# Performance work log

Measured on AMD Instinct MI355X. Metric: run time of the kernel, lower is better.

The kernel has to match this reference:

```python
import jax, jax.numpy as jnp
import numpy as np

B, T, C, H = 4, 4096, 1024, 16

def setup_inputs() -> dict:
    key = jax.random.key(0)
    k1, k2, k3, k4 = jax.random.split(key, 4)
    return {
        "x": jax.random.normal(k1, (B, T, C), dtype=jnp.float32),
        "W_attn": jax.random.normal(k2, (C, C), dtype=jnp.float32) * 0.02,
        "b_attn": jnp.zeros((C,), dtype=jnp.float32),
        "W_proj": jax.random.normal(k3, (C, C), dtype=jnp.float32) * 0.02,
        "b_proj": jnp.zeros((C,), dtype=jnp.float32),
        "temp": jnp.ones((H, 1), dtype=jnp.float32),
        "n_head": H,
    }

def reference(x, W_attn, b_attn, W_proj, b_proj, temp, n_head):
    Bb, Tt, Cc = x.shape
    D = Cc // n_head
    # c_attn (torch Linear: x @ W.T + b)
    w = x @ W_attn.T + b_attn                         # (B,T,C)
    w = w.reshape(Bb, Tt, n_head, D).transpose(0, 2, 1, 3)  # (B,H,T,D)
    # F.normalize over token axis (dim=-2), eps=1e-12
    norm = jnp.maximum(jnp.sqrt(jnp.sum(w * w, axis=-2, keepdims=True)), 1e-12)
    w_normed = w / norm
    tmp = jnp.sum(w_normed ** 2, axis=-1) * temp      # (B,H,T) * (H,1) -> (B,H,T)
    Pi = jax.nn.softmax(tmp, axis=1)                  # softmax over heads
    Pi_prob = Pi / (jnp.sum(Pi, axis=-1, keepdims=True) + 1e-8)  # (B,H,T)
    dots = jnp.einsum('bht,bhtd->bhd', Pi_prob, w ** 2)          # (B,H,D)
    attn = 1.0 / (1.0 + dots)                         # (B,H,D)
    y = -(w * Pi[..., None]) * attn[:, :, None, :]    # (B,H,T,D)
    y = y.transpose(0, 2, 1, 3).reshape(Bb, Tt, Cc)
    return y @ W_proj.T + b_proj
```

## Files before the change

kernel.cpp:

```cpp
#include <hip/hip_runtime.h>
#include <hip/hip_bf16.h>

#define BB 4
#define TT 4096
#define CC 1024
#define HH 16
#define DD 64

typedef __attribute__((ext_vector_type(8))) short short8;
typedef __attribute__((ext_vector_type(8))) __bf16 bf16x8;
typedef __attribute__((ext_vector_type(4))) float f32x4;

static __device__ __forceinline__ unsigned short f2bf(float f) {
    unsigned int u = __builtin_bit_cast(unsigned int, f);
    unsigned int r = (u + 0x7FFFu + ((u >> 16) & 1u)) >> 16;
    return (unsigned short)r;
}
static __device__ __forceinline__ float bf2f(unsigned short h) {
    return __builtin_bit_cast(float, ((unsigned int)h) << 16);
}

__global__ void k_f32_to_bf16(const float* __restrict__ src,
                              unsigned short* __restrict__ dst, int n4) {
    int i = blockIdx.x * 256 + threadIdx.x;
    if (i >= n4) return;
    float4 v = ((const float4*)src)[i];
    ushort4 o;
    o.x = f2bf(v.x); o.y = f2bf(v.y); o.z = f2bf(v.z); o.w = f2bf(v.w);
    ((ushort4*)dst)[i] = o;
}

#define GBM 256
#define GBN 256
#define GBK 32

static __device__ __forceinline__ void stage_tile32(
    const unsigned short* __restrict__ Gbase, unsigned short* lbase,
    int k0, int K, int wave, int lane)
{
    #pragma unroll
    for (int q = 0; q < 2; ++q) {
        int c = (wave * 2 + q) * 64 + lane;
        int r = c >> 2;
        int j = c & 3;
        int srcj = (j - (r >> 1)) & 3;
        const unsigned short* g = Gbase + (size_t)r * K + k0 + srcj * 8;
        __builtin_amdgcn_global_load_lds(
            (const __attribute__((address_space(1))) void*)g,
            (__attribute__((address_space(3))) void*)(lbase + (wave * 2 + q) * 512),
            16, 0, 0);
    }
}

template<int MODE>
__global__ __launch_bounds__(512, 2)
void k_gemm256(const unsigned short* __restrict__ A,
               const unsigned short* __restrict__ B,
               const float* __restrict__ bias,
               void* __restrict__ Cout,
               float* __restrict__ S,
               int M, int N, int K)
{
    __shared__ unsigned short lds[4][16384];
    const int tid  = threadIdx.x;
    const int wave = tid >> 6;
    const int lane = tid & 63;
    const int wr = wave >> 2;
    const int wc = wave & 3;
    const int fr = lane & 15;
    const int hi = lane >> 4;

    const int wg  = blockIdx.x;
    const int swz = (wg & 7) * 32 + (wg >> 3);
    const int bn  = swz & 3;
    const int bm  = swz >> 2;
    const int b   = bm >> 4;

    const unsigned short* Abase = A + (size_t)(bm * GBM) * K;
    const unsigned short* Bbase = B +
        ((size_t)((MODE == 1 ? b * N : 0) + bn * GBN)) * K;

    const int nt = K / GBK;

    const int sl   = (hi + (fr >> 1)) & 3;
    const int aoff = (wr * 128 + fr) * 32 + sl * 8;
    const int boff = 8192 + (wc * 64 + fr) * 32 + sl * 8;

    f32x4 acc[8][4] = {};

    stage_tile32(Abase, lds[0],        0,       K, wave, lane);
    stage_tile32(Bbase, lds[0] + 8192, 0,       K, wave, lane);
    stage_tile32(Abase, lds[1],        GBK,     K, wave, lane);
    stage_tile32(Bbase, lds[1] + 8192, GBK,     K, wave, lane);
    stage_tile32(Abase, lds[2],        2 * GBK, K, wave, lane);
    stage_tile32(Bbase, lds[2] + 8192, 2 * GBK, K, wave, lane);

    for (int kt = 0; kt < nt; ++kt) {
        const unsigned short* buf = lds[kt & 3];
        unsigned short* sbuf = lds[(kt + 3) & 3];
        int k3 = kt + 3; if (k3 >= nt) k3 = nt - 1;

        asm volatile("s_waitcnt vmcnt(8)" ::: "memory");
        __builtin_amdgcn_s_barrier();

        short8 af[8], bfr[4];
        #pragma unroll
        for (int i = 0; i < 4; ++i) bfr[i] = *(const short8*)&buf[boff + i * 512];
        #pragma unroll
        for (int i = 0; i < 8; ++i) af[i] = *(const short8*)&buf[aoff + i * 512];

        stage_tile32(Abase, sbuf, k3 * GBK, K, wave, lane);
        stage_tile32(Bbase, sbuf + 8192, k3 * GBK, K, wave, lane);

        __builtin_amdgcn_s_setprio(1);
        #pragma unroll
        for (int mi = 0; mi < 8; ++mi)
            #pragma unroll
            for (int ni = 0; ni < 4; ++ni)
                acc[mi][ni] = __builtin_amdgcn_mfma_f32_16x16x32_bf16(
                    __builtin_bit_cast(bf16x8, af[mi]),
                    __builtin_bit_cast(bf16x8, bfr[ni]),
                    acc[mi][ni], 0, 0, 0);
        __builtin_amdgcn_s_setprio(0);
    }

    __syncthreads();

    const int cg = fr;
    const int rg = hi * 4;
    float* sblk = (float*)&lds[0][0];
    if (MODE == 0) {
        if (tid < GBN) sblk[tid] = 0.f;
        __syncthreads();
    }
    float csum[4] = {};
    #pragma unroll
    for (int mi = 0; mi < 8; ++mi) {
        #pragma unroll
        for (int ni = 0; ni < 4; ++ni) {
            int col = bn * GBN + wc * 64 + ni * 16 + cg;
            float bv = bias[col];
            #pragma unroll
            for (int j = 0; j < 4; ++j) {
                int row = bm * GBM + wr * 128 + mi * 16 + rg + j;
                float v = acc[mi][ni][j] + bv;
                if (MODE == 0) {
                    ((unsigned short*)Cout)[(size_t)row * N + col] = f2bf(v);
                    csum[ni] += v * v;
                } else {
                    ((float*)Cout)[(size_t)row * N + col] = v;
                }
            }
        }
    }
    if (MODE == 0) {
        #pragma unroll
        for (int ni = 0; ni < 4; ++ni)
            atomicAdd(&sblk[wc * 64 + ni * 16 + cg], csum[ni]);
        __syncthreads();
        if (tid < GBN) atomicAdd(&S[b * CC + bn * GBN + tid], sblk[tid]);
    }
}

__global__ __launch_bounds__(256)
void k_row_softmax(unsigned short* __restrict__ w16, const float* __restrict__ S,
                   const float* __restrict__ temp,
                   float* __restrict__ dotsU, float* __restrict__ sumPi)
{
    __shared__ float dots_local[CC];
    __shared__ float sPi_local[HH];
    const int tid  = threadIdx.x;
    const int wave = tid >> 6;
    const int lane = tid & 63;
    const int bb   = blockIdx.x >> 7;
    const int tile = blockIdx.x & 127;

    for (int c = tid; c < CC; c += 256) dots_local[c] = 0.f;
    if (tid < HH) sPi_local[tid] = 0.f;
    __syncthreads();

    const int g3 = lane >> 3;
    const int li = lane & 7;

    float inv[2][8], tsc[2];
    #pragma unroll
    for (int q = 0; q < 2; ++q) {
        int c = q * 512 + lane * 8;
        const float4* sp = (const float4*)&S[bb * CC + c];
        float4 s0 = sp[0], s1 = sp[1];
        inv[q][0] = 1.f / fmaxf(s0.x, 1e-24f); inv[q][1] = 1.f / fmaxf(s0.y, 1e-24f);
        inv[q][2] = 1.f / fmaxf(s0.z, 1e-24f); inv[q][3] = 1.f / fmaxf(s0.w, 1e-24f);
        inv[q][4] = 1.f / fmaxf(s1.x, 1e-24f); inv[q][5] = 1.f / fmaxf(s1.y, 1e-24f);
        inv[q][6] = 1.f / fmaxf(s1.z, 1e-24f); inv[q][7] = 1.f / fmaxf(s1.w, 1e-24f);
        tsc[q] = temp[q * 8 + g3];
    }

    float dacc[2][8] = {};
    float sPiAcc[2] = {};

    for (int i = 0; i < 8; ++i) {
        int t = tile * 32 + wave * 8 + i;
        unsigned short* row = w16 + ((size_t)bb * TT + t) * CC;
        float wf[2][8];
        float pq[2];
        #pragma unroll
        for (int q = 0; q < 2; ++q) {
            short8 v = *(const short8*)&row[q * 512 + lane * 8];
            float s = 0.f;
            #pragma unroll
            for (int j = 0; j < 8; ++j) {
                wf[q][j] = bf2f((unsigned short)v[j]);
                s += wf[q][j] * wf[q][j] * inv[q][j];
            }
            pq[q] = s;
        }
        #pragma unroll
        for (int off = 1; off < 8; off <<= 1) {
            pq[0] += __shfl_xor(pq[0], off);
            pq[1] += __shfl_xor(pq[1], off);
        }
        pq[0] *= tsc[0]; pq[1] *= tsc[1];
        float mx = fmaxf(pq[0], pq[1]);
        mx = fmaxf(mx, __shfl_xor(mx, 8));
        mx = fmaxf(mx, __shfl_xor(mx, 16));
        mx = fmaxf(mx, __shfl_xor(mx, 32));
        float e0 = __expf(pq[0] - mx), e1 = __expf(pq[1] - mx);
        float ss = e0 + e1;
        ss += __shfl_xor(ss, 8);
        ss += __shfl_xor(ss, 16);
        ss += __shfl_xor(ss, 32);
        float rs = 1.f / ss;
        float piv[2] = { e0 * rs, e1 * rs };
        #pragma unroll
        for (int q = 0; q < 2; ++q) {
            short8 yo;
            #pragma unroll
            for (int j = 0; j < 8; ++j) {
                dacc[q][j] += piv[q] * wf[q][j] * wf[q][j];
                yo[j] = (short)f2bf(-wf[q][j] * piv[q]);
            }
            *(short8*)&row[q * 512 + lane * 8] = yo;
            if (li == 0) sPiAcc[q] += piv[q];
        }
    }

    #pragma unroll
    for (int q = 0; q < 2; ++q) {
        int c = q * 512 + lane * 8;
        #pragma unroll
        for (int j = 0; j < 8; ++j)
            atomicAdd(&dots_local[c + j], dacc[q][j]);
        if (li == 0) atomicAdd(&sPi_local[q * 8 + g3], sPiAcc[q]);
    }
    __syncthreads();
    for (int c = tid; c < CC; c += 256) atomicAdd(&dotsU[bb * CC + c], dots_local[c]);
    if (tid < HH) atomicAdd(&sumPi[bb * HH + tid], sPi_local[tid]);
}

__global__ void k_scale_wproj(const float* __restrict__ Wp,
                              const float* __restrict__ dotsU,
                              const float* __restrict__ sumPi,
                              unsigned short* __restrict__ out)
{
    int i = blockIdx.x * 256 + threadIdx.x;
    int bq  = i >> 18;
    int rem = i & 262143;
    int n   = rem >> 8;
    int cg  = (rem & 255) * 4;
    float4 wv = *(const float4*)&Wp[n * CC + cg];
    float4 du = *(const float4*)&dotsU[bq * CC + cg];
    float sp = sumPi[bq * HH + (cg >> 6)] + 1e-8f;
    float a0 = 1.f / (1.f + du.x / sp);
    float a1 = 1.f / (1.f + du.y / sp);
    float a2 = 1.f / (1.f + du.z / sp);
    float a3 = 1.f / (1.f + du.w / sp);
    ushort4 o;
    o.x = f2bf(wv.x * a0); o.y = f2bf(wv.y * a1);
    o.z = f2bf(wv.z * a2); o.w = f2bf(wv.w * a3);
    *(ushort4*)&out[((size_t)bq * CC + n) * CC + cg] = o;
}

extern "C" void kernel_launch(void* const* d_in, const int* in_sizes, int n_in,
                              void* d_out, int out_size, void* d_ws, size_t ws_size,
                              hipStream_t stream) {
    const float* x      = (const float*)d_in[0];
    const float* W_attn = (const float*)d_in[1];
    const float* b_attn = (const float*)d_in[2];
    const float* W_proj = (const float*)d_in[3];
    const float* b_proj = (const float*)d_in[4];
    const float* temp   = (const float*)d_in[5];

    unsigned short* xb = (unsigned short*)d_out;

    char* ws = (char*)d_ws;
    unsigned short* w16   = (unsigned short*)(ws);
    unsigned short* Wa16  = (unsigned short*)(ws + 33554432);
    unsigned short* Wp16b = (unsigned short*)(ws + 35651584);
    float* S     = (float*)(ws + 44040192);
    float* dotsU = (float*)(ws + 44056576);
    float* sumPi = (float*)(ws + 44072960);

    k_f32_to_bf16<<<dim3(16384), dim3(256), 0, stream>>>(x, xb, 4194304);
    k_f32_to_bf16<<<dim3(1024), dim3(256), 0, stream>>>(W_attn, Wa16, 262144);

    hipMemsetAsync(S, 0, 16384 + 16384 + 256, stream);

    k_gemm256<0><<<dim3(256), dim3(512), 0, stream>>>(
        xb, Wa16, b_attn, w16, S, BB * TT, CC, CC);

    k_row_softmax<<<dim3(512), dim3(256), 0, stream>>>(w16, S, temp, dotsU, sumPi);

    k_scale_wproj<<<dim3(4096), dim3(256), 0, stream>>>(W_proj, dotsU, sumPi, Wp16b);

    k_gemm256<1><<<dim3(256), dim3(512), 0, stream>>>(
        w16, Wp16b, b_proj, d_out, nullptr, BB * TT, CC, CC);
}
```

Measured before the change: 129.8 us.

## Shrink GEMM tile to 128x256 with 3-stage pipeline and fuse input conversions

Halves the GEMM M tile from 256 to 128 rows, which doubles the grid to 512 workgroups so all CUs get work. The LDS ring goes from 4 to 3 buffers and prefetch depth from 3 to 2 stages, with the wait count adjusted to match, and launch bounds now allow 4 blocks per CU. The two fp32-to-bf16 conversion launches are merged into one. The trade-off is less data reuse per tile and a shallower prefetch that may expose more memory latency.

```diff
diff --git a/kernel.cpp b/kernel.cpp
--- a/kernel.cpp
+++ b/kernel.cpp
@@ -20,21 +20,24 @@
     return __builtin_bit_cast(float, ((unsigned int)h) << 16);
 }
 
-__global__ void k_f32_to_bf16(const float* __restrict__ src,
-                              unsigned short* __restrict__ dst, int n4) {
+__global__ void k_convert2(const float* __restrict__ x, unsigned short* __restrict__ xb,
+                           const float* __restrict__ Wa, unsigned short* __restrict__ wab) {
     int i = blockIdx.x * 256 + threadIdx.x;
-    if (i >= n4) return;
-    float4 v = ((const float4*)src)[i];
+    const float* src; unsigned short* dst; int idx;
+    if (i < 4194304) { src = x;  dst = xb;  idx = i; }
+    else             { src = Wa; dst = wab; idx = i - 4194304; }
+    float4 v = ((const float4*)src)[idx];
     ushort4 o;
     o.x = f2bf(v.x); o.y = f2bf(v.y); o.z = f2bf(v.z); o.w = f2bf(v.w);
-    ((ushort4*)dst)[i] = o;
-}
-
-#define GBM 256
+    ((ushort4*)dst)[idx] = o;
+}
+
+#define GBM 128
 #define GBN 256
 #define GBK 32
-
-static __device__ __forceinline__ void stage_tile32(
+#define SLAB 12288
+
+static __device__ __forceinline__ void stage_b(
     const unsigned short* __restrict__ Gbase, unsigned short* lbase,
     int k0, int K, int wave, int lane)
 {
@@ -52,16 +55,31 @@
     }
 }
 
+static __device__ __forceinline__ void stage_a(
+    const unsigned short* __restrict__ Gbase, unsigned short* lbase,
+    int k0, int K, int wave, int lane)
+{
+    int c = wave * 64 + lane;
+    int r = c >> 2;
+    int j = c & 3;
+    int srcj = (j - (r >> 1)) & 3;
+    const unsigned short* g = Gbase + (size_t)r * K + k0 + srcj * 8;
+    __builtin_amdgcn_global_load_lds(
+        (const __attribute__((address_space(1))) void*)g,
+        (__attribute__((address_space(3))) void*)(lbase + wave * 512),
+        16, 0, 0);
+}
+
 template<int MODE>
-__global__ __launch_bounds__(512, 2)
-void k_gemm256(const unsigned short* __restrict__ A,
+__global__ __launch_bounds__(512, 4)
+void k_gemm128(const unsigned short* __restrict__ A,
                const unsigned short* __restrict__ B,
                const float* __restrict__ bias,
                void* __restrict__ Cout,
                float* __restrict__ S,
                int M, int N, int K)
 {
-    __shared__ unsigned short lds[4][16384];
+    __shared__ unsigned short lds[3][SLAB];
     const int tid  = threadIdx.x;
     const int wave = tid >> 6;
     const int lane = tid & 63;
@@ -71,10 +89,10 @@
     const int hi = lane >> 4;
 
     const int wg  = blockIdx.x;
-    const int swz = (wg & 7) * 32 + (wg >> 3);
+    const int swz = (wg & 7) * 64 + (wg >> 3);
     const int bn  = swz & 3;
     const int bm  = swz >> 2;
-    const int b   = bm >> 4;
+    const int b   = bm >> 5;
 
     const unsigned short* Abase = A + (size_t)(bm * GBM) * K;
     const unsigned short* Bbase = B +
@@ -83,38 +101,37 @@
     const int nt = K / GBK;
 
     const int sl   = (hi + (fr >> 1)) & 3;
-    const int aoff = (wr * 128 + fr) * 32 + sl * 8;
-    const int boff = 8192 + (wc * 64 + fr) * 32 + sl * 8;
-
-    f32x4 acc[8][4] = {};
-
-    stage_tile32(Abase, lds[0],        0,       K, wave, lane);
-    stage_tile32(Bbase, lds[0] + 8192, 0,       K, wave, lane);
-    stage_tile32(Abase, lds[1],        GBK,     K, wave, lane);
-    stage_tile32(Bbase, lds[1] + 8192, GBK,     K, wave, lane);
-    stage_tile32(Abase, lds[2],        2 * GBK, K, wave, lane);
-    stage_tile32(Bbase, lds[2] + 8192, 2 * GBK, K, wave, lane);
-
+    const int aoff = (wr * 64 + fr) * 32 + sl * 8;
+    const int boff = 4096 + (wc * 64 + fr) * 32 + sl * 8;
+
+    f32x4 acc[4][4] = {};
+
+    stage_a(Abase, lds[0],        0,   K, wave, lane);
+    stage_b(Bbase, lds[0] + 4096, 0,   K, wave, lane);
+    stage_a(Abase, lds[1],        GBK, K, wave, lane);
+    stage_b(Bbase, lds[1] + 4096, GBK, K, wave, lane);
+
+    int rb = 0;
     for (int kt = 0; kt < nt; ++kt) {
-        const unsigned short* buf = lds[kt & 3];
-        unsigned short* sbuf = lds[(kt + 3) & 3];
-        int k3 = kt + 3; if (k3 >= nt) k3 = nt - 1;
-
-        asm volatile("s_waitcnt vmcnt(8)" ::: "memory");
+        const unsigned short* buf = lds[rb];
+        const int wb = (rb == 0) ? 2 : rb - 1;
+        int k2 = kt + 2; if (k2 >= nt) k2 = nt - 1;
+
+        asm volatile("s_waitcnt vmcnt(3)" ::: "memory");
         __builtin_amdgcn_s_barrier();
 
-        short8 af[8], bfr[4];
+        short8 af[4], bfr[4];
         #pragma unroll
         for (int i = 0; i < 4; ++i) bfr[i] = *(const short8*)&buf[boff + i * 512];
         #pragma unroll
-        for (int i = 0; i < 8; ++i) af[i] = *(const short8*)&buf[aoff + i * 512];
-
-        stage_tile32(Abase, sbuf, k3 * GBK, K, wave, lane);
-        stage_tile32(Bbase, sbuf + 8192, k3 * GBK, K, wave, lane);
+        for (int i = 0; i < 4; ++i) af[i]  = *(const short8*)&buf[aoff + i * 512];
+
+        stage_a(Abase, lds[wb],        k2 * GBK, K, wave, lane);
+        stage_b(Bbase, lds[wb] + 4096, k2 * GBK, K, wave, lane);
 
         __builtin_amdgcn_s_setprio(1);
         #pragma unroll
-        for (int mi = 0; mi < 8; ++mi)
+        for (int mi = 0; mi < 4; ++mi)
             #pragma unroll
             for (int ni = 0; ni < 4; ++ni)
                 acc[mi][ni] = __builtin_amdgcn_mfma_f32_16x16x32_bf16(
@@ -122,6 +139,8 @@
                     __builtin_bit_cast(bf16x8, bfr[ni]),
                     acc[mi][ni], 0, 0, 0);
         __builtin_amdgcn_s_setprio(0);
+
+        rb = (rb == 2) ? 0 : rb + 1;
     }
 
     __syncthreads();
@@ -135,14 +154,14 @@
     }
     float csum[4] = {};
     #pragma unroll
-    for (int mi = 0; mi < 8; ++mi) {
+    for (int mi = 0; mi < 4; ++mi) {
         #pragma unroll
         for (int ni = 0; ni < 4; ++ni) {
             int col = bn * GBN + wc * 64 + ni * 16 + cg;
             float bv = bias[col];
             #pragma unroll
             for (int j = 0; j < 4; ++j) {
-                int row = bm * GBM + wr * 128 + mi * 16 + rg + j;
+                int row = bm * GBM + wr * 64 + mi * 16 + rg + j;
                 float v = acc[mi][ni][j] + bv;
                 if (MODE == 0) {
                     ((unsigned short*)Cout)[(size_t)row * N + col] = f2bf(v);
@@ -300,18 +319,17 @@
     float* dotsU = (float*)(ws + 44056576);
     float* sumPi = (float*)(ws + 44072960);
 
-    k_f32_to_bf16<<<dim3(16384), dim3(256), 0, stream>>>(x, xb, 4194304);
-    k_f32_to_bf16<<<dim3(1024), dim3(256), 0, stream>>>(W_attn, Wa16, 262144);
+    k_convert2<<<dim3(17408), dim3(256), 0, stream>>>(x, xb, W_attn, Wa16);
 
     hipMemsetAsync(S, 0, 16384 + 16384 + 256, stream);
 
-    k_gemm256<0><<<dim3(256), dim3(512), 0, stream>>>(
+    k_gemm128<0><<<dim3(512), dim3(512), 0, stream>>>(
         xb, Wa16, b_attn, w16, S, BB * TT, CC, CC);
 
     k_row_softmax<<<dim3(512), dim3(256), 0, stream>>>(w16, S, temp, dotsU, sumPi);
 
     k_scale_wproj<<<dim3(4096), dim3(256), 0, stream>>>(W_proj, dotsU, sumPi, Wp16b);
 
-    k_gemm256<1><<<dim3(256), dim3(512), 0, stream>>>(
+    k_gemm128<1><<<dim3(512), dim3(512), 0, stream>>>(
         w16, Wp16b, b_proj, d_out, nullptr, BB * TT, CC, CC);
 }
```

After: 135.3 us. 4.3% more time.

## Fuse fp32-to-bf16 conversion of x into first GEMM's A-tile loads

Applied to the files above, without the earlier changes.

Drops the separate kernel that converted x to bf16. The first GEMM now streams fp32 x tiles straight into LDS with a swizzled layout and converts them to bf16 in registers before the MFMAs. This removes a full read and write pass over the 64MB activation. In exchange, the GEMM A-tile traffic doubles, LDS per slab grows, and the pipeline depth drops from 4 to 3 stages, which may expose more load latency in that GEMM.

```diff
diff --git a/kernel.cpp b/kernel.cpp
--- a/kernel.cpp
+++ b/kernel.cpp
@@ -18,6 +18,12 @@
 }
 static __device__ __forceinline__ float bf2f(unsigned short h) {
     return __builtin_bit_cast(float, ((unsigned int)h) << 16);
+}
+static __device__ __forceinline__ bf16x8 cvt8(f32x4 a, f32x4 b) {
+    bf16x8 r;
+    r[0] = (__bf16)a[0]; r[1] = (__bf16)a[1]; r[2] = (__bf16)a[2]; r[3] = (__bf16)a[3];
+    r[4] = (__bf16)b[0]; r[5] = (__bf16)b[1]; r[6] = (__bf16)b[2]; r[7] = (__bf16)b[3];
+    return r;
 }
 
 __global__ void k_f32_to_bf16(const float* __restrict__ src,
@@ -34,7 +40,7 @@
 #define GBN 256
 #define GBK 32
 
-static __device__ __forceinline__ void stage_tile32(
+static __device__ __forceinline__ void stage_b16(
     const unsigned short* __restrict__ Gbase, unsigned short* lbase,
     int k0, int K, int wave, int lane)
 {
@@ -52,16 +58,37 @@
     }
 }
 
+static __device__ __forceinline__ void stage_a32(
+    const float* __restrict__ Gbase, unsigned short* lbase,
+    int k0, int K, int wave, int lane)
+{
+    #pragma unroll
+    for (int q = 0; q < 4; ++q) {
+        int c = q * 512 + wave * 64 + lane;
+        int r = c >> 3;
+        int j = c & 7;
+        int srcj = (j - r) & 7;
+        const float* g = Gbase + (size_t)r * K + k0 + srcj * 4;
+        __builtin_amdgcn_global_load_lds(
+            (const __attribute__((address_space(1))) void*)g,
+            (__attribute__((address_space(3))) void*)(lbase + (q * 512 + wave * 64) * 8),
+            16, 0, 0);
+    }
+}
+
 template<int MODE>
 __global__ __launch_bounds__(512, 2)
-void k_gemm256(const unsigned short* __restrict__ A,
+void k_gemm256(const void* __restrict__ Asrc,
                const unsigned short* __restrict__ B,
                const float* __restrict__ bias,
                void* __restrict__ Cout,
                float* __restrict__ S,
                int M, int N, int K)
 {
-    __shared__ unsigned short lds[4][16384];
+    constexpr int NSLAB  = (MODE == 0) ? 3 : 4;
+    constexpr int SLABSZ = (MODE == 0) ? 24576 : 16384;
+    constexpr int BOFF0  = (MODE == 0) ? 16384 : 8192;
+    __shared__ unsigned short lds[NSLAB][SLABSZ];
     const int tid  = threadIdx.x;
     const int wave = tid >> 6;
     const int lane = tid & 63;
@@ -76,41 +103,76 @@
     const int bm  = swz >> 2;
     const int b   = bm >> 4;
 
-    const unsigned short* Abase = A + (size_t)(bm * GBM) * K;
+    const float* Af32 = (const float*)Asrc + (size_t)(bm * GBM) * K;
+    const unsigned short* Ab16 = (const unsigned short*)Asrc + (size_t)(bm * GBM) * K;
     const unsigned short* Bbase = B +
         ((size_t)((MODE == 1 ? b * N : 0) + bn * GBN)) * K;
 
     const int nt = K / GBK;
 
-    const int sl   = (hi + (fr >> 1)) & 3;
-    const int aoff = (wr * 128 + fr) * 32 + sl * 8;
-    const int boff = 8192 + (wc * 64 + fr) * 32 + sl * 8;
+    const int slB  = (hi + (fr >> 1)) & 3;
+    const int aoff = (wr * 128 + fr) * 32 + slB * 8;
+    const int boff = BOFF0 + (wc * 64 + fr) * 32 + slB * 8;
+    const int sl0   = (2 * hi + fr) & 7;
+    const int sl1   = (2 * hi + 1 + fr) & 7;
+    const int arowf = (wr * 128 + fr) * 32;
 
     f32x4 acc[8][4] = {};
 
-    stage_tile32(Abase, lds[0],        0,       K, wave, lane);
-    stage_tile32(Bbase, lds[0] + 8192, 0,       K, wave, lane);
-    stage_tile32(Abase, lds[1],        GBK,     K, wave, lane);
-    stage_tile32(Bbase, lds[1] + 8192, GBK,     K, wave, lane);
-    stage_tile32(Abase, lds[2],        2 * GBK, K, wave, lane);
-    stage_tile32(Bbase, lds[2] + 8192, 2 * GBK, K, wave, lane);
-
+    if (MODE == 0) {
+        stage_a32(Af32, lds[0],         0,   K, wave, lane);
+        stage_b16(Bbase, lds[0] + BOFF0, 0,   K, wave, lane);
+        stage_a32(Af32, lds[1],         GBK, K, wave, lane);
+        stage_b16(Bbase, lds[1] + BOFF0, GBK, K, wave, lane);
+    } else {
+        stage_b16(Ab16, lds[0],         0,       K, wave, lane);
+        stage_b16(Bbase, lds[0] + BOFF0, 0,       K, wave, lane);
+        stage_b16(Ab16, lds[1],         GBK,     K, wave, lane);
+        stage_b16(Bbase, lds[1] + BOFF0, GBK,     K, wave, lane);
+        stage_b16(Ab16, lds[2],         2 * GBK, K, wave, lane);
+        stage_b16(Bbase, lds[2] + BOFF0, 2 * GBK, K, wave, lane);
+    }
+
+    int rb = 0;
     for (int kt = 0; kt < nt; ++kt) {
-        const unsigned short* buf = lds[kt & 3];
-        unsigned short* sbuf = lds[(kt + 3) & 3];
-        int k3 = kt + 3; if (k3 >= nt) k3 = nt - 1;
-
-        asm volatile("s_waitcnt vmcnt(8)" ::: "memory");
+        const unsigned short* buf;
+        unsigned short* sbuf;
+        int ks;
+        if (MODE == 0) {
+            buf  = lds[rb];
+            sbuf = lds[(rb == 0) ? 2 : rb - 1];
+            ks = kt + 2; if (ks >= nt) ks = nt - 1;
+            asm volatile("s_waitcnt vmcnt(6)" ::: "memory");
+        } else {
+            buf  = lds[kt & 3];
+            sbuf = lds[(kt + 3) & 3];
+            ks = kt + 3; if (ks >= nt) ks = nt - 1;
+            asm volatile("s_waitcnt vmcnt(8)" ::: "memory");
+        }
         __builtin_amdgcn_s_barrier();
 
-        short8 af[8], bfr[4];
+        bf16x8 af[8]; short8 bfr[4];
         #pragma unroll
         for (int i = 0; i < 4; ++i) bfr[i] = *(const short8*)&buf[boff + i * 512];
-        #pragma unroll
-        for (int i = 0; i < 8; ++i) af[i] = *(const short8*)&buf[aoff + i * 512];
-
-        stage_tile32(Abase, sbuf, k3 * GBK, K, wave, lane);
-        stage_tile32(Bbase, sbuf + 8192, k3 * GBK, K, wave, lane);
+        if (MODE == 0) {
+            const float* fbuf = (const float*)buf;
+            #pragma unroll
+            for (int mi = 0; mi < 8; ++mi)
+                af[mi] = cvt8(*(const f32x4*)&fbuf[arowf + mi * 512 + sl0 * 4],
+                              *(const f32x4*)&fbuf[arowf + mi * 512 + sl1 * 4]);
+        } else {
+            #pragma unroll
+            for (int mi = 0; mi < 8; ++mi)
+                af[mi] = __builtin_bit_cast(bf16x8, *(const short8*)&buf[aoff + mi * 512]);
+        }
+
+        if (MODE == 0) {
+            stage_a32(Af32, sbuf,         ks * GBK, K, wave, lane);
+            stage_b16(Bbase, sbuf + BOFF0, ks * GBK, K, wave, lane);
+        } else {
+            stage_b16(Ab16, sbuf,         ks * GBK, K, wave, lane);
+            stage_b16(Bbase, sbuf + BOFF0, ks * GBK, K, wave, lane);
+        }
 
         __builtin_amdgcn_s_setprio(1);
         #pragma unroll
@@ -118,10 +180,11 @@
             #pragma unroll
             for (int ni = 0; ni < 4; ++ni)
                 acc[mi][ni] = __builtin_amdgcn_mfma_f32_16x16x32_bf16(
-                    __builtin_bit_cast(bf16x8, af[mi]),
-                    __builtin_bit_cast(bf16x8, bfr[ni]),
+                    af[mi], __builtin_bit_cast(bf16x8, bfr[ni]),
                     acc[mi][ni], 0, 0, 0);
         __builtin_amdgcn_s_setprio(0);
+
+        rb = (rb == (NSLAB - 1)) ? 0 : rb + 1;
     }
 
     __syncthreads();
@@ -290,8 +353,6 @@
     const float* b_proj = (const float*)d_in[4];
     const float* temp   = (const float*)d_in[5];
 
-    unsigned short* xb = (unsigned short*)d_out;
-
     char* ws = (char*)d_ws;
     unsigned short* w16   = (unsigned short*)(ws);
     unsigned short* Wa16  = (unsigned short*)(ws + 33554432);
@@ -300,13 +361,12 @@
     float* dotsU = (float*)(ws + 44056576);
     float* sumPi = (float*)(ws + 44072960);
 
-    k_f32_to_bf16<<<dim3(16384), dim3(256), 0, stream>>>(x, xb, 4194304);
     k_f32_to_bf16<<<dim3(1024), dim3(256), 0, stream>>>(W_attn, Wa16, 262144);
 
     hipMemsetAsync(S, 0, 16384 + 16384 + 256, stream);
 
     k_gemm256<0><<<dim3(256), dim3(512), 0, stream>>>(
-        xb, Wa16, b_attn, w16, S, BB * TT, CC, CC);
+        x, Wa16, b_attn, w16, S, BB * TT, CC, CC);
 
     k_row_softmax<<<dim3(512), dim3(256), 0, stream>>>(w16, S, temp, dotsU, sumPi);
 
```

Result: faster. 124.5 us (-4.1%).

## Fuse x fp32-to-bf16 conversion into GEMM and shrink tiles to 128x128

Applied to the files above, without the earlier changes.

Removes the separate x fp32→bf16 conversion kernel by having the first GEMM stage fp32 tiles of x into LDS and convert them to bf16 in registers before MFMA. Both GEMMs switch from 256x256 tiles with 512 threads and a 4-stage async pipeline to 128x128 tiles with 256 threads and a single-buffer load/sync/compute loop. This saves a full read/write pass over x but gives up the multi-stage prefetch overlap, doubles A/B reloads per output, and doubles LDS traffic for the fp32 A tile.

```diff
diff --git a/kernel.cpp b/kernel.cpp
--- a/kernel.cpp
+++ b/kernel.cpp
@@ -18,6 +18,12 @@
 }
 static __device__ __forceinline__ float bf2f(unsigned short h) {
     return __builtin_bit_cast(float, ((unsigned int)h) << 16);
+}
+static __device__ __forceinline__ bf16x8 cvt8(f32x4 a, f32x4 b) {
+    bf16x8 r;
+    r[0] = (__bf16)a[0]; r[1] = (__bf16)a[1]; r[2] = (__bf16)a[2]; r[3] = (__bf16)a[3];
+    r[4] = (__bf16)b[0]; r[5] = (__bf16)b[1]; r[6] = (__bf16)b[2]; r[7] = (__bf16)b[3];
+    return r;
 }
 
 __global__ void k_f32_to_bf16(const float* __restrict__ src,
@@ -30,119 +36,134 @@
     ((ushort4*)dst)[i] = o;
 }
 
-#define GBM 256
-#define GBN 256
+#define GBM 128
+#define GBN 128
 #define GBK 32
 
-static __device__ __forceinline__ void stage_tile32(
+static __device__ __forceinline__ void stage_b16t(
     const unsigned short* __restrict__ Gbase, unsigned short* lbase,
-    int k0, int K, int wave, int lane)
+    int k0, int K, int tid)
 {
     #pragma unroll
     for (int q = 0; q < 2; ++q) {
-        int c = (wave * 2 + q) * 64 + lane;
+        int c = q * 256 + tid;
         int r = c >> 2;
         int j = c & 3;
         int srcj = (j - (r >> 1)) & 3;
         const unsigned short* g = Gbase + (size_t)r * K + k0 + srcj * 8;
         __builtin_amdgcn_global_load_lds(
             (const __attribute__((address_space(1))) void*)g,
-            (__attribute__((address_space(3))) void*)(lbase + (wave * 2 + q) * 512),
-            16, 0, 0);
+            (__attribute__((address_space(3))) void*)(lbase + c * 8), 16, 0, 0);
+    }
+}
+
+static __device__ __forceinline__ void stage_a32t(
+    const float* __restrict__ Gbase, unsigned short* lbase,
+    int k0, int K, int tid)
+{
+    #pragma unroll
+    for (int q = 0; q < 4; ++q) {
+        int c = q * 256 + tid;
+        int r = c >> 3;
+        int j = c & 7;
+        int srcj = (j - r) & 7;
+        const float* g = Gbase + (size_t)r * K + k0 + srcj * 4;
+        __builtin_amdgcn_global_load_lds(
+            (const __attribute__((address_space(1))) void*)g,
+            (__attribute__((address_space(3))) void*)(lbase + c * 8), 16, 0, 0);
     }
 }
 
 template<int MODE>
-__global__ __launch_bounds__(512, 2)
-void k_gemm256(const unsigned short* __restrict__ A,
+__global__ __launch_bounds__(256, 2)
+void k_gemm128(const void* __restrict__ Asrc,
                const unsigned short* __restrict__ B,
                const float* __restrict__ bias,
                void* __restrict__ Cout,
                float* __restrict__ S,
                int M, int N, int K)
 {
-    __shared__ unsigned short lds[4][16384];
+    constexpr int AREG = (MODE == 0) ? 8192 : 4096;
+    __shared__ unsigned short lds[AREG + 4096];
     const int tid  = threadIdx.x;
     const int wave = tid >> 6;
     const int lane = tid & 63;
-    const int wr = wave >> 2;
-    const int wc = wave & 3;
+    const int wr = wave >> 1;
+    const int wc = wave & 1;
     const int fr = lane & 15;
     const int hi = lane >> 4;
 
     const int wg  = blockIdx.x;
-    const int swz = (wg & 7) * 32 + (wg >> 3);
-    const int bn  = swz & 3;
-    const int bm  = swz >> 2;
-    const int b   = bm >> 4;
-
-    const unsigned short* Abase = A + (size_t)(bm * GBM) * K;
+    const int swz = (wg & 7) * 128 + (wg >> 3);
+    const int bn  = swz & 7;
+    const int bm  = swz >> 3;
+    const int b   = bm >> 5;
+
+    const float* Af32 = (const float*)Asrc + (size_t)(bm * GBM) * K;
+    const unsigned short* Ab16 = (const unsigned short*)Asrc + (size_t)(bm * GBM) * K;
     const unsigned short* Bbase = B +
         ((size_t)((MODE == 1 ? b * N : 0) + bn * GBN)) * K;
 
     const int nt = K / GBK;
 
-    const int sl   = (hi + (fr >> 1)) & 3;
-    const int aoff = (wr * 128 + fr) * 32 + sl * 8;
-    const int boff = 8192 + (wc * 64 + fr) * 32 + sl * 8;
-
-    f32x4 acc[8][4] = {};
-
-    stage_tile32(Abase, lds[0],        0,       K, wave, lane);
-    stage_tile32(Bbase, lds[0] + 8192, 0,       K, wave, lane);
-    stage_tile32(Abase, lds[1],        GBK,     K, wave, lane);
-    stage_tile32(Bbase, lds[1] + 8192, GBK,     K, wave, lane);
-    stage_tile32(Abase, lds[2],        2 * GBK, K, wave, lane);
-    stage_tile32(Bbase, lds[2] + 8192, 2 * GBK, K, wave, lane);
+    const int slB  = (hi + (fr >> 1)) & 3;
+    const int aoff = (wr * 64 + fr) * 32 + slB * 8;
+    const int boff = AREG + (wc * 64 + fr) * 32 + slB * 8;
+    const int sl0  = (2 * hi + fr) & 7;
+    const int sl1  = (2 * hi + 1 + fr) & 7;
+    const int arowf = (wr * 64 + fr) * 32;
+
+    f32x4 acc[4][4] = {};
 
     for (int kt = 0; kt < nt; ++kt) {
-        const unsigned short* buf = lds[kt & 3];
-        unsigned short* sbuf = lds[(kt + 3) & 3];
-        int k3 = kt + 3; if (k3 >= nt) k3 = nt - 1;
-
-        asm volatile("s_waitcnt vmcnt(8)" ::: "memory");
-        __builtin_amdgcn_s_barrier();
-
-        short8 af[8], bfr[4];
-        #pragma unroll
-        for (int i = 0; i < 4; ++i) bfr[i] = *(const short8*)&buf[boff + i * 512];
-        #pragma unroll
-        for (int i = 0; i < 8; ++i) af[i] = *(const short8*)&buf[aoff + i * 512];
-
-        stage_tile32(Abase, sbuf, k3 * GBK, K, wave, lane);
-        stage_tile32(Bbase, sbuf + 8192, k3 * GBK, K, wave, lane);
-
-        __builtin_amdgcn_s_setprio(1);
-        #pragma unroll
-        for (int mi = 0; mi < 8; ++mi)
+        const int k0 = kt * GBK;
+        if (MODE == 0) stage_a32t(Af32, lds, k0, K, tid);
+        else           stage_b16t(Ab16, lds, k0, K, tid);
+        stage_b16t(Bbase, lds + AREG, k0, K, tid);
+        __syncthreads();
+
+        bf16x8 af[4]; short8 bfr[4];
+        #pragma unroll
+        for (int i = 0; i < 4; ++i) bfr[i] = *(const short8*)&lds[boff + i * 512];
+        if (MODE == 0) {
+            const float* fbuf = (const float*)lds;
+            #pragma unroll
+            for (int mi = 0; mi < 4; ++mi)
+                af[mi] = cvt8(*(const f32x4*)&fbuf[arowf + mi * 512 + sl0 * 4],
+                              *(const f32x4*)&fbuf[arowf + mi * 512 + sl1 * 4]);
+        } else {
+            #pragma unroll
+            for (int mi = 0; mi < 4; ++mi)
+                af[mi] = __builtin_bit_cast(bf16x8, *(const short8*)&lds[aoff + mi * 512]);
+        }
+
+        #pragma unroll
+        for (int mi = 0; mi < 4; ++mi)
             #pragma unroll
             for (int ni = 0; ni < 4; ++ni)
                 acc[mi][ni] = __builtin_amdgcn_mfma_f32_16x16x32_bf16(
-                    __builtin_bit_cast(bf16x8, af[mi]),
-                    __builtin_bit_cast(bf16x8, bfr[ni]),
+                    af[mi], __builtin_bit_cast(bf16x8, bfr[ni]),
                     acc[mi][ni], 0, 0, 0);
-        __builtin_amdgcn_s_setprio(0);
-    }
-
-    __syncthreads();
+        __syncthreads();
+    }
 
     const int cg = fr;
     const int rg = hi * 4;
-    float* sblk = (float*)&lds[0][0];
+    float* sblk = (float*)&lds[0];
     if (MODE == 0) {
         if (tid < GBN) sblk[tid] = 0.f;
         __syncthreads();
     }
     float csum[4] = {};
     #pragma unroll
-    for (int mi = 0; mi < 8; ++mi) {
+    for (int mi = 0; mi < 4; ++mi) {
         #pragma unroll
         for (int ni = 0; ni < 4; ++ni) {
             int col = bn * GBN + wc * 64 + ni * 16 + cg;
             float bv = bias[col];
             #pragma unroll
             for (int j = 0; j < 4; ++j) {
-                int row = bm * GBM + wr * 128 + mi * 16 + rg + j;
+                int row = bm * GBM + wr * 64 + mi * 16 + rg + j;
                 float v = acc[mi][ni][j] + bv;
                 if (MODE == 0) {
                     ((unsigned short*)Cout)[(size_t)row * N + col] = f2bf(v);
@@ -290,8 +311,6 @@
     const float* b_proj = (const float*)d_in[4];
     const float* temp   = (const float*)d_in[5];
 
-    unsigned short* xb = (unsigned short*)d_out;
-
     char* ws = (char*)d_ws;
     unsigned short* w16   = (unsigned short*)(ws);
     unsigned short* Wa16  = (unsigned short*)(ws + 33554432);
@@ -300,18 +319,17 @@
     float* dotsU = (float*)(ws + 44056576);
     float* sumPi = (float*)(ws + 44072960);
 
-    k_f32_to_bf16<<<dim3(16384), dim3(256), 0, stream>>>(x, xb, 4194304);
     k_f32_to_bf16<<<dim3(1024), dim3(256), 0, stream>>>(W_attn, Wa16, 262144);
 
     hipMemsetAsync(S, 0, 16384 + 16384 + 256, stream);
 
-    k_gemm256<0><<<dim3(256), dim3(512), 0, stream>>>(
-        xb, Wa16, b_attn, w16, S, BB * TT, CC, CC);
+    k_gemm128<0><<<dim3(1024), dim3(256), 0, stream>>>(
+        x, Wa16, b_attn, w16, S, BB * TT, CC, CC);
 
     k_row_softmax<<<dim3(512), dim3(256), 0, stream>>>(w16, S, temp, dotsU, sumPi);
 
     k_scale_wproj<<<dim3(4096), dim3(256), 0, stream>>>(W_proj, dotsU, sumPi, Wp16b);
 
-    k_gemm256<1><<<dim3(256), dim3(512), 0, stream>>>(
+    k_gemm128<1><<<dim3(1024), dim3(256), 0, stream>>>(
         w16, Wp16b, b_proj, d_out, nullptr, BB * TT, CC, CC);
 }
```

Result: slower. 152.4 us (+17.5%).
